# Kernel optimization log

Measured on AMD Instinct MI355X. Metric: run time of the kernel, lower is better.

The kernel has to match this reference:

```python
import jax, jax.numpy as jnp
import numpy as np

N_EMBD = 256
N_HEAD = 8
BATCH = 4
SEQ = 2048
NEG_BIAS = -1000000000.0


def setup_inputs() -> dict:
    key = jax.random.key(0)
    ks = jax.random.split(key, 5)
    scale = 1.0 / np.sqrt(N_EMBD)
    x = jax.random.normal(ks[0], (BATCH, SEQ, N_EMBD), dtype=jnp.float32)
    # torch Linear weight layout: (out_features, in_features)
    Wq = jax.random.normal(ks[1], (N_EMBD * N_HEAD, N_EMBD), dtype=jnp.float32) * scale
    Wk = jax.random.normal(ks[2], (N_EMBD * N_HEAD, N_EMBD), dtype=jnp.float32) * scale
    Wv = jax.random.normal(ks[3], (N_EMBD * N_HEAD, N_EMBD), dtype=jnp.float32) * scale
    Wo = jax.random.normal(ks[4], (N_EMBD, N_EMBD * N_HEAD), dtype=jnp.float32) * scale / np.sqrt(N_HEAD)
    return {"x": x, "Wq": Wq, "Wk": Wk, "Wv": Wv, "Wo": Wo}


def reference(x, Wq, Wk, Wv, Wo):
    B, L, E = x.shape
    H, D = N_HEAD, N_EMBD  # d_head == n_embd in this module
    # projections: x @ W.T, then split heads -> (B, H, L, D)
    def proj(W):
        y = jnp.einsum('ble,fe->blf', x, W)  # (B, L, H*D)
        return y.reshape(B, L, H, D).transpose(0, 2, 1, 3)
    q, k, v = proj(Wq), proj(Wk), proj(Wv)
    scores = jnp.einsum('bhld,bhmd->bhlm', q, k) * (E ** -0.5)
    # first (non-causal) softmax over full rows
    attn = jax.nn.softmax(scores, axis=-1)
    # causal mask replaces disallowed probs with large negative bias, then softmax again
    causal = jnp.tril(jnp.ones((L, L), dtype=bool))
    attn = jnp.where(causal[None, None], attn, jnp.asarray(NEG_BIAS, attn.dtype))
    attn = jax.nn.softmax(attn, axis=-1)
    out = jnp.einsum('bhlm,bhmd->bhld', attn, v)  # (B, H, L, D)
    out = out.transpose(0, 2, 1, 3).reshape(B, L, H * D)
    return jnp.einsum('blf,ef->ble', out, Wo)  # (B, L, E)
```

## Files before the change

kernel.cpp:

```cpp
#include <hip/hip_runtime.h>
#include <stdint.h>

typedef unsigned short ushort_t;
typedef __attribute__((ext_vector_type(8))) short bf16x8;
typedef __attribute__((ext_vector_type(4))) short s16x4;
typedef __attribute__((ext_vector_type(4))) float f32x4;
typedef __attribute__((ext_vector_type(4))) unsigned short us4;

#define DEV __device__ __forceinline__

DEV ushort_t f2bf(float f) {
    unsigned int u = __float_as_uint(f);
    u += 0x7fffu + ((u >> 16) & 1u);
    return (ushort_t)(u >> 16);
}

DEV void async16(const ushort_t* g, ushort_t* l) {
    __builtin_amdgcn_global_load_lds(
        (const __attribute__((address_space(1))) void*)g,
        (__attribute__((address_space(3))) void*)l,
        16, 0, 0);
}

__global__ void convert_kernel(const float* __restrict__ x, const float* __restrict__ wq,
                               const float* __restrict__ wk, const float* __restrict__ wv,
                               const float* __restrict__ wo,
                               ushort_t* __restrict__ xb, ushort_t* __restrict__ wqb,
                               ushort_t* __restrict__ wkb, ushort_t* __restrict__ wvb,
                               ushort_t* __restrict__ wob)
{
    const int i = blockIdx.x * 256 + threadIdx.x;
    const float* src; ushort_t* dst; int off;
    if (i < 524288)      { src = x;  dst = xb;  off = i; }
    else if (i < 655360) { src = wq; dst = wqb; off = i - 524288; }
    else if (i < 786432) { src = wk; dst = wkb; off = i - 655360; }
    else if (i < 917504) { src = wv; dst = wvb; off = i - 786432; }
    else                 { src = wo; dst = wob; off = i - 917504; }
    const float4 v = ((const float4*)src)[off];
    us4 o;
    o[0] = f2bf(v.x); o[1] = f2bf(v.y); o[2] = f2bf(v.z); o[3] = f2bf(v.w);
    ((us4*)dst)[off] = o;
}

__global__ __launch_bounds__(256, 2) void gemm_qkv_kernel(
    const ushort_t* __restrict__ A, const ushort_t* __restrict__ Bm,
    void* __restrict__ C0, void* __restrict__ C1, void* __restrict__ C2)
{
    __shared__ ushort_t At[128 * 64];
    __shared__ ushort_t Bt[128 * 64];

    const int tid  = threadIdx.x;
    const int wave = tid >> 6;
    const int lane = tid & 63;
    const int quad = lane >> 4;
    const int l15  = lane & 15;
    const int mhalf = wave >> 1;
    const int nhalf = wave & 1;
    const int m0 = blockIdx.x * 128;
    const int n0 = blockIdx.y * 128;
    const int K = 256;

    f32x4 acc[4][4];
#pragma unroll
    for (int mf = 0; mf < 4; ++mf)
#pragma unroll
        for (int nf = 0; nf < 4; ++nf)
#pragma unroll
            for (int r = 0; r < 4; ++r) acc[mf][nf][r] = 0.f;

    const int crow = (lane & 7) ^ (lane >> 3);

    for (int k0 = 0; k0 < K; k0 += 64) {
        __syncthreads();
#pragma unroll
        for (int t = 0; t < 4; ++t) {
            const int row = wave * 32 + t * 8 + (lane >> 3);
            async16(A + (size_t)(m0 + row) * K + k0 + crow * 8,
                    At + (wave * 32 + t * 8) * 64 + lane * 8);
            async16(Bm + (size_t)(n0 + row) * K + k0 + crow * 8,
                    Bt + (wave * 32 + t * 8) * 64 + lane * 8);
        }
        __syncthreads();
#pragma unroll
        for (int ks = 0; ks < 2; ++ks) {
            bf16x8 af[4], bf[4];
#pragma unroll
            for (int mf = 0; mf < 4; ++mf) {
                const int ml = mhalf * 64 + mf * 16 + l15;
                const int c = (ks * 4 + quad) ^ (ml & 7);
                af[mf] = *(const bf16x8*)(At + ml * 64 + c * 8);
            }
#pragma unroll
            for (int nf = 0; nf < 4; ++nf) {
                const int nl = nhalf * 64 + nf * 16 + l15;
                const int c = (ks * 4 + quad) ^ (nl & 7);
                bf[nf] = *(const bf16x8*)(Bt + nl * 64 + c * 8);
            }
#pragma unroll
            for (int mf = 0; mf < 4; ++mf)
#pragma unroll
                for (int nf = 0; nf < 4; ++nf)
                    acc[mf][nf] = __builtin_amdgcn_mfma_f32_16x16x32_bf16(
                        af[mf], bf[nf], acc[mf][nf], 0, 0, 0);
        }
    }

    const int sel = n0 >> 11;
    if (sel == 2) {
#pragma unroll
        for (int mf = 0; mf < 4; ++mf)
#pragma unroll
            for (int nf = 0; nf < 4; ++nf) {
                const int row = m0 + mhalf * 64 + mf * 16 + quad * 4;
                const int colv = (n0 - 4096) + nhalf * 64 + nf * 16 + l15;
                const int b_ = row >> 11, l_ = row & 2047;
                const int h_ = colv >> 8, d_ = colv & 255;
                us4 pk;
#pragma unroll
                for (int r = 0; r < 4; ++r) pk[r] = f2bf(acc[mf][nf][r]);
                *(us4*)((ushort_t*)C2 +
                        (((size_t)(b_ * 8 + h_) * 256 + d_) * 2048 + l_)) = pk;
            }
    } else {
        ushort_t* dst = sel ? (ushort_t*)C1 : (ushort_t*)C0;
#pragma unroll
        for (int mf = 0; mf < 4; ++mf)
#pragma unroll
            for (int nf = 0; nf < 4; ++nf)
#pragma unroll
                for (int r = 0; r < 4; ++r) {
                    const int row = m0 + mhalf * 64 + mf * 16 + quad * 4 + r;
                    const int col = (n0 & 2047) + nhalf * 64 + nf * 16 + l15;
                    dst[(size_t)row * 2048 + col] = f2bf(acc[mf][nf][r]);
                }
    }
}

__global__ __launch_bounds__(256, 4) void gemm_out_kernel(
    const ushort_t* __restrict__ A, const ushort_t* __restrict__ Bm,
    float* __restrict__ C)
{
    __shared__ ushort_t At[64 * 64];
    __shared__ ushort_t Bt[128 * 64];

    const int tid  = threadIdx.x;
    const int wave = tid >> 6;
    const int lane = tid & 63;
    const int quad = lane >> 4;
    const int l15  = lane & 15;
    const int mhalf = wave >> 1;
    const int nhalf = wave & 1;
    const int m0 = blockIdx.x * 64;
    const int n0 = blockIdx.y * 128;

    f32x4 acc[2][4];
#pragma unroll
    for (int mf = 0; mf < 2; ++mf)
#pragma unroll
        for (int nf = 0; nf < 4; ++nf)
#pragma unroll
            for (int r = 0; r < 4; ++r) acc[mf][nf][r] = 0.f;

    const int crow = (lane & 7) ^ (lane >> 3);

    for (int k0 = 0; k0 < 2048; k0 += 64) {
        __syncthreads();
#pragma unroll
        for (int t = 0; t < 2; ++t) {
            const int row = wave * 16 + t * 8 + (lane >> 3);
            async16(A + (size_t)(m0 + row) * 2048 + k0 + crow * 8,
                    At + (wave * 16 + t * 8) * 64 + lane * 8);
        }
#pragma unroll
        for (int t = 0; t < 4; ++t) {
            const int row = wave * 32 + t * 8 + (lane >> 3);
            async16(Bm + (size_t)(n0 + row) * 2048 + k0 + crow * 8,
                    Bt + (wave * 32 + t * 8) * 64 + lane * 8);
        }
        __syncthreads();
#pragma unroll
        for (int ks = 0; ks < 2; ++ks) {
            bf16x8 af[2], bf[4];
#pragma unroll
            for (int mf = 0; mf < 2; ++mf) {
                const int ml = mhalf * 32 + mf * 16 + l15;
                const int c = (ks * 4 + quad) ^ (ml & 7);
                af[mf] = *(const bf16x8*)(At + ml * 64 + c * 8);
            }
#pragma unroll
            for (int nf = 0; nf < 4; ++nf) {
                const int nl = nhalf * 64 + nf * 16 + l15;
                const int c = (ks * 4 + quad) ^ (nl & 7);
                bf[nf] = *(const bf16x8*)(Bt + nl * 64 + c * 8);
            }
#pragma unroll
            for (int mf = 0; mf < 2; ++mf)
#pragma unroll
                for (int nf = 0; nf < 4; ++nf)
                    acc[mf][nf] = __builtin_amdgcn_mfma_f32_16x16x32_bf16(
                        af[mf], bf[nf], acc[mf][nf], 0, 0, 0);
        }
    }

#pragma unroll
    for (int mf = 0; mf < 2; ++mf)
#pragma unroll
        for (int nf = 0; nf < 4; ++nf)
#pragma unroll
            for (int r = 0; r < 4; ++r) {
                const int row = m0 + mhalf * 32 + mf * 16 + quad * 4 + r;
                const int col = n0 + nhalf * 64 + nf * 16 + l15;
                C[(size_t)row * 256 + col] = acc[mf][nf][r];
            }
}

__global__ __launch_bounds__(256, 4) void pass1_kernel(
    const ushort_t* __restrict__ q_ws, const ushort_t* __restrict__ k_ws,
    float* __restrict__ rz_ws)
{
    __shared__ ushort_t Kt[64 * 256];
    __shared__ float zred[2][64];

    const float SCALE = 0.0625f;
    const int tid  = threadIdx.x;
    const int wave = tid >> 6;
    const int lane = tid & 63;
    const int quad = lane >> 4;
    const int l15  = lane & 15;
    const int ihalf = wave >> 1;
    const int jhalf = wave & 1;

    const int g  = blockIdx.x;
    const int bh = ((g >> 8) << 3) | (g & 7);
    const int it = (g >> 3) & 31;
    const int b = bh >> 3, h = bh & 7;
    const int i0 = it * 64;

    const size_t qkbase = (size_t)b * 2048 * 2048 + (size_t)h * 256;

    bf16x8 qf[2][8];
#pragma unroll
    for (int ng = 0; ng < 2; ++ng) {
        const int i_l = ihalf * 32 + ng * 16 + l15;
        const ushort_t* qr = q_ws + qkbase + (size_t)(i0 + i_l) * 2048;
#pragma unroll
        for (int ks = 0; ks < 8; ++ks)
            qf[ng][ks] = *(const bf16x8*)(qr + ks * 32 + quad * 8);
    }

    float z[2] = {0.f, 0.f};

    for (int jt = 0; jt < 32; ++jt) {
        const int j0 = jt * 64;
        __syncthreads();
        {
            const ushort_t* kb = k_ws + qkbase + (size_t)j0 * 2048;
#pragma unroll
            for (int t = 0; t < 8; ++t) {
                const int row = wave * 16 + t * 2 + (lane >> 5);
                const int c = (lane & 31) ^ (row & 7);
                async16(kb + (size_t)row * 2048 + c * 8,
                        Kt + (wave * 16 + t * 2) * 256 + lane * 8);
            }
        }
        __syncthreads();

        f32x4 sacc[2][2];
#pragma unroll
        for (int a = 0; a < 2; ++a)
#pragma unroll
            for (int c = 0; c < 2; ++c)
#pragma unroll
                for (int r = 0; r < 4; ++r) sacc[a][c][r] = 0.f;

#pragma unroll
        for (int ks = 0; ks < 8; ++ks) {
            bf16x8 af[2];
#pragma unroll
            for (int mg = 0; mg < 2; ++mg) {
                const int j_l = jhalf * 32 + mg * 16 + l15;
                const int c = (ks * 4 + quad) ^ (j_l & 7);
                af[mg] = *(const bf16x8*)(Kt + j_l * 256 + c * 8);
            }
#pragma unroll
            for (int mg = 0; mg < 2; ++mg)
#pragma unroll
                for (int ng = 0; ng < 2; ++ng)
                    sacc[mg][ng] = __builtin_amdgcn_mfma_f32_16x16x32_bf16(
                        af[mg], qf[ng][ks], sacc[mg][ng], 0, 0, 0);
        }

#pragma unroll
        for (int ng = 0; ng < 2; ++ng)
#pragma unroll
            for (int mg = 0; mg < 2; ++mg)
#pragma unroll
                for (int r = 0; r < 4; ++r)
                    z[ng] += __expf(sacc[mg][ng][r] * SCALE);
    }

#pragma unroll
    for (int ng = 0; ng < 2; ++ng) {
        z[ng] += __shfl_xor(z[ng], 16);
        z[ng] += __shfl_xor(z[ng], 32);
    }
    __syncthreads();
    if (quad == 0) {
#pragma unroll
        for (int ng = 0; ng < 2; ++ng) {
            const int i_l = ihalf * 32 + ng * 16 + l15;
            zred[jhalf][i_l] = z[ng];
        }
    }
    __syncthreads();
    if (tid < 64)
        rz_ws[(size_t)bh * 2048 + i0 + tid] = 1.0f / (zred[0][tid] + zred[1][tid]);
}

__global__ __launch_bounds__(256, 2) void pass2_kernel(
    const ushort_t* __restrict__ q_ws, const ushort_t* __restrict__ k_ws,
    const ushort_t* __restrict__ vt_ws, const float* __restrict__ rz_ws,
    ushort_t* __restrict__ attn_out)
{
    __shared__ ushort_t smem[36864];
    ushort_t* Kt = smem;
    ushort_t* Vt = smem + 16384;
    ushort_t* Wt = smem + 32768;

    const float SCALE = 0.0625f;
    const int tid  = threadIdx.x;
    const int wave = tid >> 6;
    const int lane = tid & 63;
    const int quad = lane >> 4;
    const int l15  = lane & 15;

    const int g  = blockIdx.x;
    const int bh = ((g >> 8) << 3) | (g & 7);
    const int it = 31 - ((g >> 3) & 31);
    const int b = bh >> 3, h = bh & 7;
    const int i0 = it * 64;

    const size_t qkbase = (size_t)b * 2048 * 2048 + (size_t)h * 256;

    bf16x8 qf[8];
    {
        const ushort_t* qr = q_ws + qkbase + (size_t)(i0 + wave * 16 + l15) * 2048;
#pragma unroll
        for (int ks = 0; ks < 8; ++ks)
            qf[ks] = *(const bf16x8*)(qr + ks * 32 + quad * 8);
    }
    const float rz = rz_ws[(size_t)bh * 2048 + i0 + wave * 16 + l15];

    f32x4 oacc[16];
#pragma unroll
    for (int nf = 0; nf < 16; ++nf)
#pragma unroll
        for (int r = 0; r < 4; ++r) oacc[nf][r] = 0.f;
    float den = 0.f;

    ushort_t* Wp = Wt + wave * 1024;

    for (int jt = 0; jt <= it; ++jt) {
        const int j0 = jt * 64;
        const bool diag = (jt == it);
        __syncthreads();
        {
            const ushort_t* kb = k_ws + qkbase + (size_t)j0 * 2048;
#pragma unroll
            for (int t = 0; t < 8; ++t) {
                const int row = wave * 16 + t * 2 + (lane >> 5);
                const int c = (lane & 31) ^ (row & 7);
                async16(kb + (size_t)row * 2048 + c * 8,
                        Kt + (wave * 16 + t * 2) * 256 + lane * 8);
            }
            const ushort_t* vb = vt_ws + (size_t)bh * 256 * 2048 + j0;
#pragma unroll
            for (int t = 0; t < 8; ++t) {
                const int row = wave * 64 + t * 8 + (lane >> 3);
                const int c = (lane & 7) ^ (row & 7);
                async16(vb + (size_t)row * 2048 + c * 8,
                        Vt + (wave * 64 + t * 8) * 64 + lane * 8);
            }
        }
        __syncthreads();

        const int mgmax = diag ? wave : 3;

        f32x4 sacc[4];
#pragma unroll
        for (int mg = 0; mg < 4; ++mg)
#pragma unroll
            for (int r = 0; r < 4; ++r) sacc[mg][r] = 0.f;

#pragma unroll
        for (int ks = 0; ks < 8; ++ks) {
#pragma unroll
            for (int mg = 0; mg < 4; ++mg) {
                if (mg > mgmax) continue;
                const int c = (ks * 4 + quad) ^ (l15 & 7);
                const bf16x8 af = *(const bf16x8*)(Kt + (mg * 16 + l15) * 256 + c * 8);
                sacc[mg] = __builtin_amdgcn_mfma_f32_16x16x32_bf16(
                    af, qf[ks], sacc[mg], 0, 0, 0);
            }
        }

#pragma unroll
        for (int mg = 0; mg < 4; ++mg) {
            us4 wp;
            if (mg <= mgmax) {
#pragma unroll
                for (int r = 0; r < 4; ++r) {
                    const float p = __expf(sacc[mg][r] * SCALE) * rz;
                    float w = __expf(p);
                    if (diag && (mg * 16 + quad * 4 + r > wave * 16 + l15)) w = 0.f;
                    den += w;
                    wp[r] = f2bf(w);
                }
            } else {
                wp[0] = 0; wp[1] = 0; wp[2] = 0; wp[3] = 0;
            }
            const int c = (mg * 4 + quad) ^ l15;
            *(us4*)(Wp + l15 * 64 + c * 4) = wp;
        }

        const int ksmax = diag ? (wave >> 1) : 1;
#pragma unroll
        for (int ks = 0; ks < 2; ++ks) {
            if (ks > ksmax) continue;
            const s16x4 lo = *(const s16x4*)(Wp + l15 * 64 + ((ks * 8 + quad * 2)     ^ l15) * 4);
            const s16x4 hi = *(const s16x4*)(Wp + l15 * 64 + ((ks * 8 + quad * 2 + 1) ^ l15) * 4);
            union { s16x4 h[2]; bf16x8 v; } u;
            u.h[0] = lo; u.h[1] = hi;
            const bf16x8 aw = u.v;
#pragma unroll
            for (int nf = 0; nf < 16; ++nf) {
                const int d = nf * 16 + l15;
                const int c = (ks * 4 + quad) ^ (d & 7);
                const bf16x8 bv = *(const bf16x8*)(Vt + d * 64 + c * 8);
                oacc[nf] = __builtin_amdgcn_mfma_f32_16x16x32_bf16(
                    aw, bv, oacc[nf], 0, 0, 0);
            }
        }
    }

    den += __shfl_xor(den, 16);
    den += __shfl_xor(den, 32);
    if (quad == 0) ((float*)Wp)[l15] = den;
    const float* dW = (const float*)Wp;
#pragma unroll
    for (int r = 0; r < 4; ++r) {
        const int il = quad * 4 + r;
        const float rd = 1.0f / dW[il];
        ushort_t* orow = attn_out + qkbase + (size_t)(i0 + wave * 16 + il) * 2048;
#pragma unroll
        for (int nf = 0; nf < 16; ++nf)
            orow[nf * 16 + l15] = f2bf(oacc[nf][r] * rd);
    }
}

extern "C" void kernel_launch(void* const* d_in, const int* in_sizes, int n_in,
                              void* d_out, int out_size, void* d_ws, size_t ws_size,
                              hipStream_t stream) {
    const float* x  = (const float*)d_in[0];
    const float* Wq = (const float*)d_in[1];
    const float* Wk = (const float*)d_in[2];
    const float* Wv = (const float*)d_in[3];
    const float* Wo = (const float*)d_in[4];

    char* ws = (char*)d_ws;
    ushort_t* xb    = (ushort_t*)(ws);
    ushort_t* wqb   = (ushort_t*)(ws + 4194304);
    ushort_t* wkb   = (ushort_t*)(ws + 5242880);
    ushort_t* wvb   = (ushort_t*)(ws + 6291456);
    ushort_t* wob   = (ushort_t*)(ws + 7340032);
    ushort_t* q_ws  = (ushort_t*)(ws + 8388608);
    ushort_t* k_ws  = (ushort_t*)(ws + 41943040);
    ushort_t* vt_ws = (ushort_t*)(ws + 75497472);
    ushort_t* ao_ws = (ushort_t*)(ws + 109051904);
    float*    rz_ws = (float*)   (ws + 142606336);

    convert_kernel<<<4096, 256, 0, stream>>>(x, Wq, Wk, Wv, Wo, xb, wqb, wkb, wvb, wob);

    gemm_qkv_kernel<<<dim3(64, 48), 256, 0, stream>>>(xb, wqb, q_ws, k_ws, vt_ws);

    pass1_kernel<<<1024, 256, 0, stream>>>(q_ws, k_ws, rz_ws);
    pass2_kernel<<<1024, 256, 0, stream>>>(q_ws, k_ws, vt_ws, rz_ws, ao_ws);

    gemm_out_kernel<<<dim3(128, 2), 256, 0, stream>>>(ao_ws, wob, (float*)d_out);
}
```

Before: 370.4 us.

## Register-prefetch K/V tiles with smaller 32-key tiles and 2x2 wave split

Measured after the change: 794.9 us. 115% more time.

```diff
diff --git a/kernel.cpp b/kernel.cpp
--- a/kernel.cpp
+++ b/kernel.cpp
@@ -20,6 +20,10 @@
         (const __attribute__((address_space(1))) void*)g,
         (__attribute__((address_space(3))) void*)l,
         16, 0, 0);
+}
+
+DEV void barrier_lgkm() {
+    __asm__ volatile("s_waitcnt lgkmcnt(0)\n\ts_barrier" ::: "memory");
 }
 
 __global__ void convert_kernel(const float* __restrict__ x, const float* __restrict__ wq,
@@ -214,11 +218,11 @@
             }
 }
 
-__global__ __launch_bounds__(256, 4) void pass1_kernel(
+__global__ __launch_bounds__(256, 3) void pass1_kernel(
     const ushort_t* __restrict__ q_ws, const ushort_t* __restrict__ k_ws,
     float* __restrict__ rz_ws)
 {
-    __shared__ ushort_t Kt[64 * 256];
+    __shared__ ushort_t Kt[32 * 256];
     __shared__ float zred[2][64];
 
     const float SCALE = 0.0625f;
@@ -248,55 +252,50 @@
             qf[ng][ks] = *(const bf16x8*)(qr + ks * 32 + quad * 8);
     }
 
+    const int srow = wave * 8 + (lane >> 5);
+    const int scol = (lane & 31) ^ (srow & 7);
+    const ushort_t* kbase = k_ws + qkbase + (size_t)srow * 2048 + scol * 8;
+    uint4 kst[4];
+#pragma unroll
+    for (int t = 0; t < 4; ++t)
+        kst[t] = *(const uint4*)(kbase + (size_t)(t * 2) * 2048);
+
     float z[2] = {0.f, 0.f};
 
-    for (int jt = 0; jt < 32; ++jt) {
-        const int j0 = jt * 64;
-        __syncthreads();
-        {
-            const ushort_t* kb = k_ws + qkbase + (size_t)j0 * 2048;
-#pragma unroll
-            for (int t = 0; t < 8; ++t) {
-                const int row = wave * 16 + t * 2 + (lane >> 5);
-                const int c = (lane & 31) ^ (row & 7);
-                async16(kb + (size_t)row * 2048 + c * 8,
-                        Kt + (wave * 16 + t * 2) * 256 + lane * 8);
-            }
-        }
-        __syncthreads();
-
-        f32x4 sacc[2][2];
-#pragma unroll
-        for (int a = 0; a < 2; ++a)
-#pragma unroll
-            for (int c = 0; c < 2; ++c)
-#pragma unroll
-                for (int r = 0; r < 4; ++r) sacc[a][c][r] = 0.f;
+    for (int jt = 0; jt < 64; ++jt) {
+        barrier_lgkm();
+#pragma unroll
+        for (int t = 0; t < 4; ++t)
+            *(uint4*)(Kt + (wave * 8 + t * 2) * 256 + lane * 8) = kst[t];
+        if (jt < 63) {
+            const ushort_t* kb = kbase + (size_t)(jt + 1) * 32 * 2048;
+#pragma unroll
+            for (int t = 0; t < 4; ++t)
+                kst[t] = *(const uint4*)(kb + (size_t)(t * 2) * 2048);
+        }
+        barrier_lgkm();
+
+        f32x4 sacc[2];
+#pragma unroll
+        for (int ng = 0; ng < 2; ++ng)
+#pragma unroll
+            for (int r = 0; r < 4; ++r) sacc[ng][r] = 0.f;
 
 #pragma unroll
         for (int ks = 0; ks < 8; ++ks) {
-            bf16x8 af[2];
-#pragma unroll
-            for (int mg = 0; mg < 2; ++mg) {
-                const int j_l = jhalf * 32 + mg * 16 + l15;
-                const int c = (ks * 4 + quad) ^ (j_l & 7);
-                af[mg] = *(const bf16x8*)(Kt + j_l * 256 + c * 8);
-            }
-#pragma unroll
-            for (int mg = 0; mg < 2; ++mg)
-#pragma unroll
-                for (int ng = 0; ng < 2; ++ng)
-                    sacc[mg][ng] = __builtin_amdgcn_mfma_f32_16x16x32_bf16(
-                        af[mg], qf[ng][ks], sacc[mg][ng], 0, 0, 0);
-        }
-
+            const int j_l = jhalf * 16 + l15;
+            const int c = (ks * 4 + quad) ^ (j_l & 7);
+            const bf16x8 af = *(const bf16x8*)(Kt + j_l * 256 + c * 8);
+#pragma unroll
+            for (int ng = 0; ng < 2; ++ng)
+                sacc[ng] = __builtin_amdgcn_mfma_f32_16x16x32_bf16(
+                    af, qf[ng][ks], sacc[ng], 0, 0, 0);
+        }
 #pragma unroll
         for (int ng = 0; ng < 2; ++ng)
 #pragma unroll
-            for (int mg = 0; mg < 2; ++mg)
-#pragma unroll
-                for (int r = 0; r < 4; ++r)
-                    z[ng] += __expf(sacc[mg][ng][r] * SCALE);
+            for (int r = 0; r < 4; ++r)
+                z[ng] += __expf(sacc[ng][r] * SCALE);
     }
 
 #pragma unroll
@@ -307,10 +306,8 @@
     __syncthreads();
     if (quad == 0) {
 #pragma unroll
-        for (int ng = 0; ng < 2; ++ng) {
-            const int i_l = ihalf * 32 + ng * 16 + l15;
-            zred[jhalf][i_l] = z[ng];
-        }
+        for (int ng = 0; ng < 2; ++ng)
+            zred[jhalf][ihalf * 32 + ng * 16 + l15] = z[ng];
     }
     __syncthreads();
     if (tid < 64)
@@ -322,10 +319,10 @@
     const ushort_t* __restrict__ vt_ws, const float* __restrict__ rz_ws,
     ushort_t* __restrict__ attn_out)
 {
-    __shared__ ushort_t smem[36864];
-    ushort_t* Kt = smem;
-    ushort_t* Vt = smem + 16384;
-    ushort_t* Wt = smem + 32768;
+    __shared__ ushort_t Kt[32 * 256];
+    __shared__ ushort_t Vt[256 * 32];
+    __shared__ ushort_t Wt[64 * 32];
+    __shared__ float dred[128];
 
     const float SCALE = 0.0625f;
     const int tid  = threadIdx.x;
@@ -333,128 +330,168 @@
     const int lane = tid & 63;
     const int quad = lane >> 4;
     const int l15  = lane & 15;
+    const int ihalf = wave >> 1;
+    const int jhalf = wave & 1;
 
     const int g  = blockIdx.x;
     const int bh = ((g >> 8) << 3) | (g & 7);
     const int it = 31 - ((g >> 3) & 31);
     const int b = bh >> 3, h = bh & 7;
     const int i0 = it * 64;
+    const int jtmax = 2 * it + 1;
 
     const size_t qkbase = (size_t)b * 2048 * 2048 + (size_t)h * 256;
-
-    bf16x8 qf[8];
-    {
-        const ushort_t* qr = q_ws + qkbase + (size_t)(i0 + wave * 16 + l15) * 2048;
+    const size_t vtbase = (size_t)bh * 256 * 2048;
+
+    bf16x8 qf[2][8];
+#pragma unroll
+    for (int ng = 0; ng < 2; ++ng) {
+        const int i_l = ihalf * 32 + ng * 16 + l15;
+        const ushort_t* qr = q_ws + qkbase + (size_t)(i0 + i_l) * 2048;
 #pragma unroll
         for (int ks = 0; ks < 8; ++ks)
-            qf[ks] = *(const bf16x8*)(qr + ks * 32 + quad * 8);
-    }
-    const float rz = rz_ws[(size_t)bh * 2048 + i0 + wave * 16 + l15];
-
-    f32x4 oacc[16];
-#pragma unroll
-    for (int nf = 0; nf < 16; ++nf)
-#pragma unroll
-        for (int r = 0; r < 4; ++r) oacc[nf][r] = 0.f;
-    float den = 0.f;
-
-    ushort_t* Wp = Wt + wave * 1024;
-
-    for (int jt = 0; jt <= it; ++jt) {
-        const int j0 = jt * 64;
-        const bool diag = (jt == it);
-        __syncthreads();
-        {
-            const ushort_t* kb = k_ws + qkbase + (size_t)j0 * 2048;
-#pragma unroll
-            for (int t = 0; t < 8; ++t) {
-                const int row = wave * 16 + t * 2 + (lane >> 5);
-                const int c = (lane & 31) ^ (row & 7);
-                async16(kb + (size_t)row * 2048 + c * 8,
-                        Kt + (wave * 16 + t * 2) * 256 + lane * 8);
-            }
-            const ushort_t* vb = vt_ws + (size_t)bh * 256 * 2048 + j0;
-#pragma unroll
-            for (int t = 0; t < 8; ++t) {
-                const int row = wave * 64 + t * 8 + (lane >> 3);
-                const int c = (lane & 7) ^ (row & 7);
-                async16(vb + (size_t)row * 2048 + c * 8,
-                        Vt + (wave * 64 + t * 8) * 64 + lane * 8);
-            }
-        }
-        __syncthreads();
-
-        const int mgmax = diag ? wave : 3;
-
-        f32x4 sacc[4];
-#pragma unroll
-        for (int mg = 0; mg < 4; ++mg)
-#pragma unroll
-            for (int r = 0; r < 4; ++r) sacc[mg][r] = 0.f;
-
-#pragma unroll
-        for (int ks = 0; ks < 8; ++ks) {
-#pragma unroll
-            for (int mg = 0; mg < 4; ++mg) {
-                if (mg > mgmax) continue;
-                const int c = (ks * 4 + quad) ^ (l15 & 7);
-                const bf16x8 af = *(const bf16x8*)(Kt + (mg * 16 + l15) * 256 + c * 8);
-                sacc[mg] = __builtin_amdgcn_mfma_f32_16x16x32_bf16(
-                    af, qf[ks], sacc[mg], 0, 0, 0);
-            }
-        }
-
-#pragma unroll
-        for (int mg = 0; mg < 4; ++mg) {
-            us4 wp;
-            if (mg <= mgmax) {
+            qf[ng][ks] = *(const bf16x8*)(qr + ks * 32 + quad * 8);
+    }
+    float rzrow[2];
+#pragma unroll
+    for (int ng = 0; ng < 2; ++ng)
+        rzrow[ng] = rz_ws[(size_t)bh * 2048 + i0 + ihalf * 32 + ng * 16 + l15];
+
+    const int krow = wave * 8 + (lane >> 5);
+    const int kcol = (lane & 31) ^ (krow & 7);
+    const ushort_t* kbase = k_ws + qkbase + (size_t)krow * 2048 + kcol * 8;
+    const int vrow = wave * 64 + (lane >> 2);
+    const int vcol = (lane & 3) ^ (vrow & 3);
+    const ushort_t* vbase = vt_ws + vtbase + (size_t)vrow * 2048 + vcol * 8;
+
+    uint4 kst[4], vst[4];
+#pragma unroll
+    for (int t = 0; t < 4; ++t) {
+        kst[t] = *(const uint4*)(kbase + (size_t)(t * 2) * 2048);
+        vst[t] = *(const uint4*)(vbase + (size_t)(t * 16) * 2048);
+    }
+
+    f32x4 oacc[2][8];
+#pragma unroll
+    for (int mg = 0; mg < 2; ++mg)
+#pragma unroll
+        for (int nf = 0; nf < 8; ++nf)
+#pragma unroll
+            for (int r = 0; r < 4; ++r) oacc[mg][nf][r] = 0.f;
+    float den[2] = {0.f, 0.f};
+
+    const int iblo = it * 4 + ihalf * 2;
+
+    for (int jt = 0; jt <= jtmax; ++jt) {
+        barrier_lgkm();
+#pragma unroll
+        for (int t = 0; t < 4; ++t) {
+            *(uint4*)(Kt + (wave * 8 + t * 2) * 256 + lane * 8) = kst[t];
+            *(uint4*)(Vt + (wave * 64 + t * 16) * 32 + lane * 8) = vst[t];
+        }
+        if (jt < jtmax) {
+            const ushort_t* kb = kbase + (size_t)(jt + 1) * 32 * 2048;
+            const ushort_t* vb = vbase + (size_t)(jt + 1) * 32;
+#pragma unroll
+            for (int t = 0; t < 4; ++t) {
+                kst[t] = *(const uint4*)(kb + (size_t)(t * 2) * 2048);
+                vst[t] = *(const uint4*)(vb + (size_t)(t * 16) * 2048);
+            }
+        }
+        barrier_lgkm();
+
+        const int jb16 = jt * 2 + jhalf;
+        if (jb16 <= iblo + 1) {
+            f32x4 sacc[2];
+#pragma unroll
+            for (int ng = 0; ng < 2; ++ng)
+#pragma unroll
+                for (int r = 0; r < 4; ++r) sacc[ng][r] = 0.f;
+#pragma unroll
+            for (int ks = 0; ks < 8; ++ks) {
+                const int j_l = jhalf * 16 + l15;
+                const int c = (ks * 4 + quad) ^ (j_l & 7);
+                const bf16x8 af = *(const bf16x8*)(Kt + j_l * 256 + c * 8);
+#pragma unroll
+                for (int ng = 0; ng < 2; ++ng)
+                    sacc[ng] = __builtin_amdgcn_mfma_f32_16x16x32_bf16(
+                        af, qf[ng][ks], sacc[ng], 0, 0, 0);
+            }
+            const bool need_mask = (jb16 >= iblo);
+#pragma unroll
+            for (int ng = 0; ng < 2; ++ng) {
+                const int di = (i0 + ihalf * 32 + ng * 16 + l15)
+                             - (jt * 32 + jhalf * 16 + quad * 4);
+                us4 wp;
 #pragma unroll
                 for (int r = 0; r < 4; ++r) {
-                    const float p = __expf(sacc[mg][r] * SCALE) * rz;
+                    const float p = __expf(sacc[ng][r] * SCALE) * rzrow[ng];
                     float w = __expf(p);
-                    if (diag && (mg * 16 + quad * 4 + r > wave * 16 + l15)) w = 0.f;
-                    den += w;
+                    if (need_mask && (r > di)) w = 0.f;
+                    den[ng] += w;
                     wp[r] = f2bf(w);
                 }
-            } else {
-                wp[0] = 0; wp[1] = 0; wp[2] = 0; wp[3] = 0;
-            }
-            const int c = (mg * 4 + quad) ^ l15;
-            *(us4*)(Wp + l15 * 64 + c * 4) = wp;
-        }
-
-        const int ksmax = diag ? (wave >> 1) : 1;
-#pragma unroll
-        for (int ks = 0; ks < 2; ++ks) {
-            if (ks > ksmax) continue;
-            const s16x4 lo = *(const s16x4*)(Wp + l15 * 64 + ((ks * 8 + quad * 2)     ^ l15) * 4);
-            const s16x4 hi = *(const s16x4*)(Wp + l15 * 64 + ((ks * 8 + quad * 2 + 1) ^ l15) * 4);
-            union { s16x4 h[2]; bf16x8 v; } u;
-            u.h[0] = lo; u.h[1] = hi;
-            const bf16x8 aw = u.v;
-#pragma unroll
-            for (int nf = 0; nf < 16; ++nf) {
-                const int d = nf * 16 + l15;
-                const int c = (ks * 4 + quad) ^ (d & 7);
-                const bf16x8 bv = *(const bf16x8*)(Vt + d * 64 + c * 8);
-                oacc[nf] = __builtin_amdgcn_mfma_f32_16x16x32_bf16(
-                    aw, bv, oacc[nf], 0, 0, 0);
-            }
-        }
-    }
-
-    den += __shfl_xor(den, 16);
-    den += __shfl_xor(den, 32);
-    if (quad == 0) ((float*)Wp)[l15] = den;
-    const float* dW = (const float*)Wp;
-#pragma unroll
-    for (int r = 0; r < 4; ++r) {
-        const int il = quad * 4 + r;
-        const float rd = 1.0f / dW[il];
-        ushort_t* orow = attn_out + qkbase + (size_t)(i0 + wave * 16 + il) * 2048;
-#pragma unroll
-        for (int nf = 0; nf < 16; ++nf)
-            orow[nf * 16 + l15] = f2bf(oacc[nf][r] * rd);
+                const int row = ihalf * 32 + ng * 16 + l15;
+                const int c = (jhalf * 4 + quad) ^ (l15 & 7);
+                *(us4*)(Wt + row * 32 + c * 4) = wp;
+            }
+        } else {
+            const us4 zz = {0, 0, 0, 0};
+#pragma unroll
+            for (int ng = 0; ng < 2; ++ng) {
+                const int row = ihalf * 32 + ng * 16 + l15;
+                const int c = (jhalf * 4 + quad) ^ (l15 & 7);
+                *(us4*)(Wt + row * 32 + c * 4) = zz;
+            }
+        }
+        barrier_lgkm();
+
+        if (jt <= it * 2 + ihalf) {
+            bf16x8 aw[2];
+#pragma unroll
+            for (int mg = 0; mg < 2; ++mg) {
+                const int row = ihalf * 32 + mg * 16 + l15;
+                const s16x4 lo = *(const s16x4*)(Wt + row * 32 + ((2 * quad)     ^ (l15 & 7)) * 4);
+                const s16x4 hi = *(const s16x4*)(Wt + row * 32 + ((2 * quad + 1) ^ (l15 & 7)) * 4);
+                union { s16x4 h[2]; bf16x8 v; } u;
+                u.h[0] = lo; u.h[1] = hi;
+                aw[mg] = u.v;
+            }
+#pragma unroll
+            for (int nf = 0; nf < 8; ++nf) {
+                const int d = jhalf * 128 + nf * 16 + l15;
+                const int c = quad ^ (d & 3);
+                const bf16x8 bv = *(const bf16x8*)(Vt + d * 32 + c * 8);
+                oacc[0][nf] = __builtin_amdgcn_mfma_f32_16x16x32_bf16(aw[0], bv, oacc[0][nf], 0, 0, 0);
+                oacc[1][nf] = __builtin_amdgcn_mfma_f32_16x16x32_bf16(aw[1], bv, oacc[1][nf], 0, 0, 0);
+            }
+        }
+    }
+
+#pragma unroll
+    for (int ng = 0; ng < 2; ++ng) {
+        den[ng] += __shfl_xor(den[ng], 16);
+        den[ng] += __shfl_xor(den[ng], 32);
+    }
+    __syncthreads();
+    if (quad == 0) {
+#pragma unroll
+        for (int ng = 0; ng < 2; ++ng)
+            dred[(ihalf * 2 + jhalf) * 32 + ng * 16 + l15] = den[ng];
+    }
+    __syncthreads();
+#pragma unroll
+    for (int mg = 0; mg < 2; ++mg) {
+#pragma unroll
+        for (int r = 0; r < 4; ++r) {
+            const int il = mg * 16 + quad * 4 + r;
+            const float dt = dred[(ihalf * 2) * 32 + il] + dred[(ihalf * 2 + 1) * 32 + il];
+            const float rd = 1.0f / dt;
+            ushort_t* orow = attn_out + qkbase + (size_t)(i0 + ihalf * 32 + il) * 2048;
+#pragma unroll
+            for (int nf = 0; nf < 8; ++nf)
+                orow[jhalf * 128 + nf * 16 + l15] = f2bf(oacc[mg][nf][r] * rd);
+        }
     }
 }
 
```
